# Performance work log

Measured on AMD Instinct MI355X. Metric: run time of the kernel, lower is better.

Reference implementation:

```python
import jax, jax.numpy as jnp
import numpy as np

BATCH = 2048
DIMS = [256, 256, 256, 128]  # input, hidden, hidden, output
N_ATOMS = 4  # identity, sin, tanh, square


def setup_inputs() -> dict:
    key = jax.random.key(0)
    ks = jax.random.split(key, 8)
    inp = {"x": jax.random.normal(ks[0], (BATCH, DIMS[0]), dtype=jnp.float32)}
    for li in range(3):
        out_d, in_d = DIMS[li + 1], DIMS[li]
        inp[f"W{li}"] = jax.random.normal(ks[1 + li], (out_d, in_d), dtype=jnp.float32) * 0.1
        inp[f"b{li}"] = jnp.zeros((out_d,), dtype=jnp.float32)
        inp[f"f_idx{li}"] = jax.random.randint(ks[4 + li], (out_d, in_d), 0, N_ATOMS, dtype=jnp.int32)
    return inp


def _w_eff(W, idx):
    # per-element atom nonlinearity selected by idx: [identity, sin, tanh, square]
    atoms = jnp.stack([W, jnp.sin(W), jnp.tanh(W), W * W], axis=0)  # [A, out, in]
    return jnp.take_along_axis(atoms, idx[None].astype(jnp.int32), axis=0)[0]


def reference(x, W0, b0, W1, b1, W2, b2, f_idx0, f_idx1, f_idx2):
    layers = [(W0, b0, f_idx0), (W1, b1, f_idx1), (W2, b2, f_idx2)]
    h = x
    n = len(layers)
    for li, (W, b, idx) in enumerate(layers):
        We = _w_eff(W, idx)                       # [out, in]
        z = h[:, None, :] * We[None, :, :]        # [batch, out, in]
        gz = z if li == n - 1 else jnp.tanh(z)    # g_fixed='tanh' on hidden layers
        h = gz.sum(axis=-1) + b[None, :]          # [batch, out]
    return h
```

## Files before the change

### kernel.cpp

```cpp
#include <hip/hip_runtime.h>
#include <math.h>


#define RB 2

__device__ __forceinline__ float fast_rcp(float x)  { return __builtin_amdgcn_rcpf(x); }
__device__ __forceinline__ float fast_exp2(float x) { return __builtin_amdgcn_exp2f(x); }

#define SC  2.885390081777927f
#define INV (1.0f / 2.885390081777927f)
#define INV2PI 0.15915494309189535f

__global__ void weff_kernel(const float* __restrict__ W0, const int* __restrict__ I0,
                            const float* __restrict__ W1, const int* __restrict__ I1,
                            const float* __restrict__ W2, const int* __restrict__ I2,
                            float* __restrict__ ws) {
    int tid = blockIdx.x * blockDim.x + threadIdx.x;
    const float* W; const int* I; float* out; int outd; int e;
    if (tid < 65536)        { W = W0; I = I0; out = ws;          outd = 256; e = tid; }
    else if (tid < 131072)  { W = W1; I = I1; out = ws + 65536;  outd = 256; e = tid - 65536; }
    else if (tid < 163840)  { W = W2; I = I2; out = ws + 131072; outd = 128; e = tid - 131072; }
    else return;
    int o = e >> 8;
    int i = e & 255;
    float w = W[e];
    int idx = I[e];
    float sn = __builtin_amdgcn_sinf(w * INV2PI);
    float th = 1.0f - 2.0f * fast_rcp(fast_exp2(w * SC) + 1.0f);
    float sq = w * w;
    float v = (idx == 1) ? sn : (idx == 2) ? th : (idx == 3) ? sq : w;
    out[(i >> 2) * (outd * 4) + o * 4 + (i & 3)] = v;
}

__global__ __launch_bounds__(256) void mlp_kernel(
    const float* __restrict__ x,  const float* __restrict__ b0,
    const float* __restrict__ b1, const float* __restrict__ b2,
    const float* __restrict__ ws, float* __restrict__ out) {
    const float4* We0 = (const float4*)ws;
    const float4* We1 = (const float4*)(ws + 65536);
    const float4* We2 = (const float4*)(ws + 131072);

    __shared__ __align__(16) float hA[RB][256];
    __shared__ __align__(16) float hB[RB][256];

    const int t = threadIdx.x;
    const int row0 = blockIdx.x * RB;

#pragma unroll
    for (int k = 0; k < RB; k++)
        hA[k][t] = x[(row0 + k) * 256 + t] * SC;
    __syncthreads();

    {
        const float bias = b0[t];
        float acc0 = 0.f, acc1 = 0.f;
#pragma unroll 4
        for (int ic = 0; ic < 64; ic++) {
            float4 w  = We0[ic * 256 + t];
            float4 h0 = *(const float4*)&hA[0][ic * 4];
            float4 h1 = *(const float4*)&hA[1][ic * 4];
            acc0 += fast_rcp(fast_exp2(h0.x * w.x) + 1.f);
            acc0 += fast_rcp(fast_exp2(h0.y * w.y) + 1.f);
            acc0 += fast_rcp(fast_exp2(h0.z * w.z) + 1.f);
            acc0 += fast_rcp(fast_exp2(h0.w * w.w) + 1.f);
            acc1 += fast_rcp(fast_exp2(h1.x * w.x) + 1.f);
            acc1 += fast_rcp(fast_exp2(h1.y * w.y) + 1.f);
            acc1 += fast_rcp(fast_exp2(h1.z * w.z) + 1.f);
            acc1 += fast_rcp(fast_exp2(h1.w * w.w) + 1.f);
        }
        hB[0][t] = (256.0f - 2.0f * acc0 + bias) * SC;
        hB[1][t] = (256.0f - 2.0f * acc1 + bias) * SC;
        __syncthreads();
    }

    {
        const float bias = b1[t];
        float acc0 = 0.f, acc1 = 0.f;
#pragma unroll 4
        for (int ic = 0; ic < 64; ic++) {
            float4 w  = We1[ic * 256 + t];
            float4 h0 = *(const float4*)&hB[0][ic * 4];
            float4 h1 = *(const float4*)&hB[1][ic * 4];
            acc0 += fast_rcp(fast_exp2(h0.x * w.x) + 1.f);
            acc0 += fast_rcp(fast_exp2(h0.y * w.y) + 1.f);
            acc0 += fast_rcp(fast_exp2(h0.z * w.z) + 1.f);
            acc0 += fast_rcp(fast_exp2(h0.w * w.w) + 1.f);
            acc1 += fast_rcp(fast_exp2(h1.x * w.x) + 1.f);
            acc1 += fast_rcp(fast_exp2(h1.y * w.y) + 1.f);
            acc1 += fast_rcp(fast_exp2(h1.z * w.z) + 1.f);
            acc1 += fast_rcp(fast_exp2(h1.w * w.w) + 1.f);
        }
        hA[0][t] = (256.0f - 2.0f * acc0 + bias) * SC;
        hA[1][t] = (256.0f - 2.0f * acc1 + bias) * SC;
        __syncthreads();
    }

    {
        const int o = t & 127;
        const int r = t >> 7;
        float acc = 0.f;
#pragma unroll 4
        for (int ic = 0; ic < 64; ic++) {
            float4 w = We2[ic * 128 + o];
            float4 h = *(const float4*)&hA[r][ic * 4];
            acc += h.x * w.x + h.y * w.y + h.z * w.z + h.w * w.w;
        }
        out[(row0 + r) * 128 + o] = acc * INV + b2[o];
    }
}

extern "C" void kernel_launch(void* const* d_in, const int* in_sizes, int n_in,
                              void* d_out, int out_size, void* d_ws, size_t ws_size,
                              hipStream_t stream) {
    const float* x  = (const float*)d_in[0];
    const float* W0 = (const float*)d_in[1];
    const float* b0 = (const float*)d_in[2];
    const int*   I0 = (const int*)  d_in[3];
    const float* W1 = (const float*)d_in[4];
    const float* b1 = (const float*)d_in[5];
    const int*   I1 = (const int*)  d_in[6];
    const float* W2 = (const float*)d_in[7];
    const float* b2 = (const float*)d_in[8];
    const int*   I2 = (const int*)  d_in[9];
    float* ws  = (float*)d_ws;
    float* out = (float*)d_out;

    weff_kernel<<<640, 256, 0, stream>>>(W0, I0, W1, I1, W2, I2, ws);
    mlp_kernel<<<2048 / RB, 256, 0, stream>>>(x, b0, b1, b2, ws, out);
}
```

Baseline: 130.0 us.

## Use 1024-thread blocks with one row per thread group and split-K final layer

```diff
diff --git a/kernel.cpp b/kernel.cpp
--- a/kernel.cpp
+++ b/kernel.cpp
@@ -1,8 +1,6 @@
 #include <hip/hip_runtime.h>
 #include <math.h>
 
-
-#define RB 2
 
 __device__ __forceinline__ float fast_rcp(float x)  { return __builtin_amdgcn_rcpf(x); }
 __device__ __forceinline__ float fast_exp2(float x) { return __builtin_amdgcn_exp2f(x); }
@@ -32,7 +30,7 @@
     out[(i >> 2) * (outd * 4) + o * 4 + (i & 3)] = v;
 }
 
-__global__ __launch_bounds__(256) void mlp_kernel(
+__global__ __launch_bounds__(1024, 8) void mlp_kernel(
     const float* __restrict__ x,  const float* __restrict__ b0,
     const float* __restrict__ b1, const float* __restrict__ b2,
     const float* __restrict__ ws, float* __restrict__ out) {
@@ -40,72 +38,66 @@
     const float4* We1 = (const float4*)(ws + 65536);
     const float4* We2 = (const float4*)(ws + 131072);
 
-    __shared__ __align__(16) float hA[RB][256];
-    __shared__ __align__(16) float hB[RB][256];
+    __shared__ __align__(16) float hA[4][256];
+    __shared__ __align__(16) float hB[4][256];
 
     const int t = threadIdx.x;
-    const int row0 = blockIdx.x * RB;
+    const int r = t >> 8;
+    const int o = t & 255;
+    const int row0 = blockIdx.x * 4;
 
-#pragma unroll
-    for (int k = 0; k < RB; k++)
-        hA[k][t] = x[(row0 + k) * 256 + t] * SC;
+    hA[r][o] = x[(row0 + r) * 256 + o] * SC;
     __syncthreads();
 
     {
-        const float bias = b0[t];
-        float acc0 = 0.f, acc1 = 0.f;
+        const float bias = b0[o];
+        float acc = 0.f;
 #pragma unroll 4
         for (int ic = 0; ic < 64; ic++) {
-            float4 w  = We0[ic * 256 + t];
-            float4 h0 = *(const float4*)&hA[0][ic * 4];
-            float4 h1 = *(const float4*)&hA[1][ic * 4];
-            acc0 += fast_rcp(fast_exp2(h0.x * w.x) + 1.f);
-            acc0 += fast_rcp(fast_exp2(h0.y * w.y) + 1.f);
-            acc0 += fast_rcp(fast_exp2(h0.z * w.z) + 1.f);
-            acc0 += fast_rcp(fast_exp2(h0.w * w.w) + 1.f);
-            acc1 += fast_rcp(fast_exp2(h1.x * w.x) + 1.f);
-            acc1 += fast_rcp(fast_exp2(h1.y * w.y) + 1.f);
-            acc1 += fast_rcp(fast_exp2(h1.z * w.z) + 1.f);
-            acc1 += fast_rcp(fast_exp2(h1.w * w.w) + 1.f);
+            float4 w = We0[ic * 256 + o];
+            float4 h = *(const float4*)&hA[r][ic * 4];
+            acc += fast_rcp(fast_exp2(h.x * w.x) + 1.f);
+            acc += fast_rcp(fast_exp2(h.y * w.y) + 1.f);
+            acc += fast_rcp(fast_exp2(h.z * w.z) + 1.f);
+            acc += fast_rcp(fast_exp2(h.w * w.w) + 1.f);
         }
-        hB[0][t] = (256.0f - 2.0f * acc0 + bias) * SC;
-        hB[1][t] = (256.0f - 2.0f * acc1 + bias) * SC;
+        hB[r][o] = (256.0f - 2.0f * acc + bias) * SC;
         __syncthreads();
     }
 
     {
-        const float bias = b1[t];
-        float acc0 = 0.f, acc1 = 0.f;
+        const float bias = b1[o];
+        float acc = 0.f;
 #pragma unroll 4
         for (int ic = 0; ic < 64; ic++) {
-            float4 w  = We1[ic * 256 + t];
-            float4 h0 = *(const float4*)&hB[0][ic * 4];
-            float4 h1 = *(const float4*)&hB[1][ic * 4];
-            acc0 += fast_rcp(fast_exp2(h0.x * w.x) + 1.f);
-            acc0 += fast_rcp(fast_exp2(h0.y * w.y) + 1.f);
-            acc0 += fast_rcp(fast_exp2(h0.z * w.z) + 1.f);
-            acc0 += fast_rcp(fast_exp2(h0.w * w.w) + 1.f);
-            acc1 += fast_rcp(fast_exp2(h1.x * w.x) + 1.f);
-            acc1 += fast_rcp(fast_exp2(h1.y * w.y) + 1.f);
-            acc1 += fast_rcp(fast_exp2(h1.z * w.z) + 1.f);
-            acc1 += fast_rcp(fast_exp2(h1.w * w.w) + 1.f);
+            float4 w = We1[ic * 256 + o];
+            float4 h = *(const float4*)&hB[r][ic * 4];
+            acc += fast_rcp(fast_exp2(h.x * w.x) + 1.f);
+            acc += fast_rcp(fast_exp2(h.y * w.y) + 1.f);
+            acc += fast_rcp(fast_exp2(h.z * w.z) + 1.f);
+            acc += fast_rcp(fast_exp2(h.w * w.w) + 1.f);
         }
-        hA[0][t] = (256.0f - 2.0f * acc0 + bias) * SC;
-        hA[1][t] = (256.0f - 2.0f * acc1 + bias) * SC;
+        hA[r][o] = (256.0f - 2.0f * acc + bias) * SC;
         __syncthreads();
     }
 
     {
-        const int o = t & 127;
-        const int r = t >> 7;
+        const int o2 = t & 127;
+        const int kk = (t >> 7) & 1;
         float acc = 0.f;
 #pragma unroll 4
-        for (int ic = 0; ic < 64; ic++) {
-            float4 w = We2[ic * 128 + o];
+        for (int ic = kk * 32; ic < kk * 32 + 32; ic++) {
+            float4 w = We2[ic * 128 + o2];
             float4 h = *(const float4*)&hA[r][ic * 4];
             acc += h.x * w.x + h.y * w.y + h.z * w.z + h.w * w.w;
         }
-        out[(row0 + r) * 128 + o] = acc * INV + b2[o];
+        hB[r][kk * 128 + o2] = acc;
+        __syncthreads();
+        if (t < 512) {
+            int rr = t >> 7, oo = t & 127;
+            out[(row0 + rr) * 128 + oo] =
+                (hB[rr][oo] + hB[rr][128 + oo]) * INV + b2[oo];
+        }
     }
 }
 
@@ -126,5 +118,5 @@
     float* out = (float*)d_out;
 
     weff_kernel<<<640, 256, 0, stream>>>(W0, I0, W1, I1, W2, I2, ws);
-    mlp_kernel<<<2048 / RB, 256, 0, stream>>>(x, b0, b1, b2, ws, out);
+    mlp_kernel<<<512, 1024, 0, stream>>>(x, b0, b1, b2, ws, out);
 }
```

New measurement: 135.3 us. 4.0% more time.
